# Kernel tuning notes

Measured on AMD Instinct MI355X. Metric: run time of the kernel, lower is better.

The kernel has to match this reference:

```python
import jax, jax.numpy as jnp
import numpy as np

L, D, H, HD, FF, T = 8, 1024, 16, 64, 4096, 4096
SCALE = 1.4 / np.sqrt(float(L))  # muP residual scale: scale_depth/sqrt(num_hidden_layers)
THETA, EPS = 10000.0, 1e-5


def _rms(x, w):
    return x * jax.lax.rsqrt(jnp.mean(x * x, axis=-1, keepdims=True) + EPS) * w


def _rope(x, cos, sin):
    # rotate-half RoPE on last dim; cos/sin: [HD//2]
    x1, x2 = jnp.split(x, 2, axis=-1)
    return jnp.concatenate([x1 * cos - x2 * sin, x1 * sin + x2 * cos], axis=-1)


def setup_inputs() -> dict:
    key = jax.random.key(0)
    ks = jax.random.split(key, 10)
    nrm = lambda k, shape, s=1.0: jax.random.normal(k, shape, dtype=jnp.float32) * s
    inp = {"embed": nrm(ks[0], (1, 1, D))}
    ck = jax.random.split(ks[1], 2 * L)
    for i in range(L):
        inp[f"k{i}"] = nrm(ck[2 * i], (1, H, T, HD))
        inp[f"v{i}"] = nrm(ck[2 * i + 1], (1, H, T, HD))
    inp["ln1_w"] = jnp.ones((L, D), jnp.float32)
    inp["ln2_w"] = jnp.ones((L, D), jnp.float32)
    inp["norm_w"] = jnp.ones((D,), jnp.float32)
    w = 0.02
    inp["Wq"] = nrm(ks[2], (L, D, D), w)
    inp["Wk"] = nrm(ks[3], (L, D, D), w)
    inp["Wv"] = nrm(ks[4], (L, D, D), w)
    inp["Wo"] = nrm(ks[5], (L, D, D), w)
    inp["Wg"] = nrm(ks[6], (L, D, FF), w)
    inp["Wu"] = nrm(ks[7], (L, D, FF), w)
    inp["Wd"] = nrm(ks[8], (L, FF, D), w)
    inp["position"] = T  # decode position == current cache length
    return inp


def reference(embed, position, k0, v0, k1, v1, k2, v2, k3, v3, k4, v4, k5, v5, k6, v6, k7, v7,
              ln1_w, ln2_w, norm_w, Wq, Wk, Wv, Wo, Wg, Wu, Wd):
    caches = [(k0, v0), (k1, v1), (k2, v2), (k3, v3), (k4, v4), (k5, v5), (k6, v6), (k7, v7)]
    inv_freq = 1.0 / (THETA ** (jnp.arange(0, HD, 2, dtype=jnp.float32) / HD))  # [HD//2]
    ang = jnp.asarray(position, jnp.float32) * inv_freq
    cos, sin = jnp.cos(ang), jnp.sin(ang)
    hidden = embed  # [1,1,D]
    new_caches = []
    for i in range(L):
        residual = hidden
        h = _rms(hidden, ln1_w[i])
        q = (h @ Wq[i]).reshape(1, 1, H, HD).transpose(0, 2, 1, 3)   # [1,H,1,HD]
        kn = (h @ Wk[i]).reshape(1, 1, H, HD).transpose(0, 2, 1, 3)
        vn = (h @ Wv[i]).reshape(1, 1, H, HD).transpose(0, 2, 1, 3)
        q, kn = _rope(q, cos, sin), _rope(kn, cos, sin)
        kc = jnp.concatenate([caches[i][0], kn], axis=2)  # [1,H,T+1,HD]
        vc = jnp.concatenate([caches[i][1], vn], axis=2)
        new_caches.append((kc, vc))
        scores = jnp.einsum('bhqd,bhkd->bhqk', q, kc) / np.sqrt(float(HD))
        attn = jax.nn.softmax(scores, axis=-1)
        o = jnp.einsum('bhqk,bhkd->bhqd', attn, vc).transpose(0, 2, 1, 3).reshape(1, 1, D) @ Wo[i]
        hidden = residual + o * SCALE
        residual = hidden
        h = _rms(hidden, ln2_w[i])
        m = (jax.nn.silu(h @ Wg[i]) * (h @ Wu[i])) @ Wd[i]
        hidden = residual + m * SCALE
    out = [_rms(hidden, norm_w)]
    for kc, vc in new_caches:
        out.extend([kc, vc])
    return tuple(out)
```

## Files before the change

### kernel.cpp

```cpp
#include <hip/hip_runtime.h>
#include <stdint.h>

#define D_ 1024
#define H_ 16
#define HD_ 64
#define FF_ 4096
#define T_ 4096
#define TC_ 4097
#define CHUNK_ 128
#define NCH_ 32
#define NV_ 9
#define LAYERS_ 8

#define WS_QKV 0
#define WS_GU 3072
#define WS_HID 11264
#define WS_PART 12288

static constexpr float SCALE_ = 0.49497474683058327f;
static constexpr float EPS_ = 1e-5f;

typedef float nf4 __attribute__((ext_vector_type(4)));

__device__ __forceinline__ float wave_sum(float v) {
    #pragma unroll
    for (int off = 32; off; off >>= 1) v += __shfl_down(v, off, 64);
    return v;
}
__device__ __forceinline__ float wave_max(float v) {
    #pragma unroll
    for (int off = 32; off; off >>= 1) v = fmaxf(v, __shfl_down(v, off, 64));
    return v;
}

__device__ __forceinline__ void rms_to_sm(const float* __restrict__ hid,
                                          const float* __restrict__ lnw,
                                          float* hn, float* wred, int t)
{
    float4 hv = ((const float4*)hid)[t];
    float ssq = hv.x*hv.x + hv.y*hv.y + hv.z*hv.z + hv.w*hv.w;
    ssq = wave_sum(ssq);
    if ((t & 63) == 0) wred[t >> 6] = ssq;
    __syncthreads();
    float rms = rsqrtf((wred[0] + wred[1] + wred[2] + wred[3]) * (1.0f / D_) + EPS_);
    float4 lw = ((const float4*)lnw)[t];
    hn[4*t+0] = hv.x * rms * lw.x;
    hn[4*t+1] = hv.y * rms * lw.y;
    hn[4*t+2] = hv.z * rms * lw.z;
    hn[4*t+3] = hv.w * rms * lw.w;
    __syncthreads();
}

template<int RT>
__device__ __forceinline__ void gemv_tile(const float* __restrict__ hsrc,
                                          const float* __restrict__ W, int ncols,
                                          int rowbase, int colbase, float scale,
                                          float* __restrict__ dst, float4* red4, int t)
{
    constexpr int RPG = RT / 8;
    int cg = t & 31, rg = t >> 5;
    int row0 = rowbase + rg * RPG;
    const float* Wp = W + (size_t)row0 * ncols + colbase + cg * 4;
    float4 acc = make_float4(0.f, 0.f, 0.f, 0.f);
    #pragma unroll
    for (int r = 0; r < RPG; ++r) {
        float hs = hsrc[row0 + r];
        float4 w4 = *(const float4*)(Wp + (size_t)r * ncols);
        acc.x += hs*w4.x; acc.y += hs*w4.y; acc.z += hs*w4.z; acc.w += hs*w4.w;
    }
    red4[t] = acc;
    __syncthreads();
    if (t < 32) {
        float4 s = red4[t];
        #pragma unroll
        for (int g = 1; g < 8; ++g) {
            float4 r4 = red4[t + 32*g];
            s.x += r4.x; s.y += r4.y; s.z += r4.z; s.w += r4.w;
        }
        float* d = dst + colbase + t*4;
        atomicAdd(d+0, scale*s.x);
        atomicAdd(d+1, scale*s.y);
        atomicAdd(d+2, scale*s.z);
        atomicAdd(d+3, scale*s.w);
    }
    __syncthreads();
}

__global__ void k_init(const float* __restrict__ embed, float* __restrict__ hid,
                       float* __restrict__ accQKV) {
    int t = threadIdx.x;
    ((float4*)hid)[t] = ((const float4*)embed)[t];
    for (int i = t; i < 3072; i += 256) accQKV[i] = 0.f;
}

template<int NCOLS, int RT>
__global__ void k_rms_gemv(const float* __restrict__ hidden, const float* __restrict__ lnw,
                           const float* __restrict__ W0, const float* __restrict__ W1,
                           const float* __restrict__ W2, float* __restrict__ out)
{
    int t = threadIdx.x;
    __shared__ float hn[D_];
    __shared__ float wred[4];
    __shared__ float4 red4s[256];
    rms_to_sm(hidden, lnw, hn, wred, t);
    const float* W = (blockIdx.z == 0) ? W0 : (blockIdx.z == 1 ? W1 : W2);
    gemv_tile<RT>(hn, W, NCOLS, blockIdx.y*RT, blockIdx.x*128, 1.f,
                  out + (size_t)blockIdx.z * NCOLS, red4s, t);
}

__global__ void k_attn_f(const float* __restrict__ kcache, const float* __restrict__ vcache,
                         const float* __restrict__ qkv, const int* __restrict__ posp,
                         float* __restrict__ kc_out, float* __restrict__ vc_out,
                         float* __restrict__ part)
{
    int c = blockIdx.x, h = blockIdx.y, t = threadIdx.x;
    __shared__ float qr[64], kr[64], sc[132], wr2[8];
    __shared__ float4 red4[256];
    if (t < 32) {
        float pos = (float)(*posp);
        float inv = expf(-(float)t * (9.210340371976184f / 32.0f));
        float ang = pos * inv;
        float cs = cosf(ang), sn = sinf(ang);
        float q1 = qkv[h*64 + t], q2 = qkv[h*64 + t + 32];
        qr[t] = q1*cs - q2*sn; qr[t+32] = q1*sn + q2*cs;
        float k1 = qkv[1024 + h*64 + t], k2 = qkv[1024 + h*64 + t + 32];
        kr[t] = k1*cs - k2*sn; kr[t+32] = k1*sn + k2*cs;
    }

    int kstart = c * CHUNK_;
    int nk = (c == NCH_-1) ? (TC_ - kstart) : CHUNK_;
    int d4 = (t & 15) * 4;
    int kl0 = t >> 4;

    nf4 vreg[NV_];
    #pragma unroll
    for (int j = 0; j < NV_; ++j) {
        int kl = kl0 + 16 * j;
        if (kl < nk) {
            int key = kstart + kl;
            if (key < T_)
                vreg[j] = __builtin_nontemporal_load((const nf4*)(vcache + ((size_t)h*T_ + key)*HD_ + d4));
            else
                vreg[j] = *(const nf4*)(qkv + 2048 + h*64 + d4);
        }
    }

    __syncthreads();
    nf4 qv = *(const nf4*)&qr[d4];
    #pragma unroll
    for (int j = 0; j < NV_; ++j) {
        int kl = kl0 + 16 * j;
        if (kl < nk) {
            int key = kstart + kl;
            nf4 kv;
            if (key < T_) kv = __builtin_nontemporal_load((const nf4*)(kcache + ((size_t)h*T_ + key)*HD_ + d4));
            else          kv = *(const nf4*)&kr[d4];
            float pd = qv.x*kv.x + qv.y*kv.y + qv.z*kv.z + qv.w*kv.w;
            pd += __shfl_down(pd, 8, 16);
            pd += __shfl_down(pd, 4, 16);
            pd += __shfl_down(pd, 2, 16);
            pd += __shfl_down(pd, 1, 16);
            if ((t & 15) == 0) sc[kl] = pd * 0.125f;
            __builtin_nontemporal_store(kv, (nf4*)(kc_out + ((size_t)h*TC_ + key)*HD_ + d4));
        }
    }
    #pragma unroll
    for (int j = 0; j < NV_; ++j) {
        int kl = kl0 + 16 * j;
        if (kl < nk) {
            int key = kstart + kl;
            __builtin_nontemporal_store(vreg[j], (nf4*)(vc_out + ((size_t)h*TC_ + key)*HD_ + d4));
        }
    }
    __syncthreads();
    float m = (t < nk) ? sc[t] : -INFINITY;
    m = wave_max(m);
    if ((t & 63) == 0) wr2[t >> 6] = m;
    __syncthreads();
    m = fmaxf(fmaxf(wr2[0], wr2[1]), fmaxf(wr2[2], wr2[3]));
    float e = 0.f;
    if (t < nk) { e = __expf(sc[t] - m); sc[t] = e; }
    float s = wave_sum(e);
    if ((t & 63) == 0) wr2[4 + (t >> 6)] = s;
    __syncthreads();
    float* pb = part + ((size_t)h*NCH_ + c)*66;
    if (t == 0) { pb[0] = m; pb[1] = wr2[4]+wr2[5]+wr2[6]+wr2[7]; }
    __syncthreads();
    float4 acc = make_float4(0.f, 0.f, 0.f, 0.f);
    #pragma unroll
    for (int j = 0; j < NV_; ++j) {
        int kl = kl0 + 16 * j;
        if (kl < nk) {
            float w = sc[kl];
            acc.x += w*vreg[j].x; acc.y += w*vreg[j].y;
            acc.z += w*vreg[j].z; acc.w += w*vreg[j].w;
        }
    }
    red4[t] = acc;
    __syncthreads();
    if (t < 16) {
        float4 s4 = red4[t];
        #pragma unroll
        for (int g = 1; g < 16; ++g) {
            float4 r4 = red4[t + 16*g];
            s4.x += r4.x; s4.y += r4.y; s4.z += r4.z; s4.w += r4.w;
        }
        pb[2 + t*4 + 0] = s4.x;
        pb[2 + t*4 + 1] = s4.y;
        pb[2 + t*4 + 2] = s4.z;
        pb[2 + t*4 + 3] = s4.w;
    }
}

__global__ void k_wo(const float* __restrict__ part, const float* __restrict__ Wo,
                     float* __restrict__ hidden, float* __restrict__ accGU)
{
    int h = blockIdx.y, t = threadIdx.x;
    if (blockIdx.x == 0 && blockIdx.y == 0)
        for (int i = t; i < 2*FF_; i += 256) accGU[i] = 0.f;
    __shared__ float oh[64];
    __shared__ float4 red4s[256];
    if (t < 64) {
        const float* pb = part + (size_t)h * NCH_ * 66;
        float M = -INFINITY;
        for (int c = 0; c < NCH_; ++c) M = fmaxf(M, pb[c*66]);
        float S = 0.f, O = 0.f;
        for (int c = 0; c < NCH_; ++c) {
            float e = __expf(pb[c*66] - M);
            S += pb[c*66 + 1] * e;
            O += pb[c*66 + 2 + t] * e;
        }
        oh[t] = O / S;
    }
    __syncthreads();
    gemv_tile<64>(oh - h*64, Wo, D_, h*64, blockIdx.x*128, SCALE_, hidden, red4s, t);
}

__global__ void k_down(const float* __restrict__ gu, const float* __restrict__ Wd,
                       float* __restrict__ hidden, float* __restrict__ accQKV)
{
    int t = threadIdx.x;
    if (blockIdx.x == 0 && blockIdx.y == 0)
        for (int i = t; i < 3072; i += 256) accQKV[i] = 0.f;
    __shared__ float act[128];
    __shared__ float4 red4s[256];
    int rowbase = blockIdx.y * 128;
    if (t < 128) {
        float g = gu[rowbase + t];
        float u = gu[FF_ + rowbase + t];
        act[t] = g / (1.f + __expf(-g)) * u;
    }
    __syncthreads();
    gemv_tile<128>(act - rowbase, Wd, D_, rowbase, blockIdx.x*128, SCALE_, hidden, red4s, t);
}

__global__ void k_final(const float* __restrict__ hidden, const float* __restrict__ nw,
                        float* __restrict__ out)
{
    int t = threadIdx.x;
    __shared__ float wred[4];
    float4 hv = ((const float4*)hidden)[t];
    float ssq = hv.x*hv.x + hv.y*hv.y + hv.z*hv.z + hv.w*hv.w;
    ssq = wave_sum(ssq);
    if ((t & 63) == 0) wred[t >> 6] = ssq;
    __syncthreads();
    float rms = rsqrtf((wred[0] + wred[1] + wred[2] + wred[3]) * (1.0f / D_) + EPS_);
    float4 w = ((const float4*)nw)[t];
    float4 ob;
    ob.x = hv.x * rms * w.x; ob.y = hv.y * rms * w.y;
    ob.z = hv.z * rms * w.z; ob.w = hv.w * rms * w.w;
    ((float4*)out)[t] = ob;
}

static const int ROLE_SIZES[28] = {
    1024,
    4194304,4194304,4194304,4194304,4194304,4194304,4194304,4194304,
    4194304,4194304,4194304,4194304,4194304,4194304,4194304,4194304,
    8192, 8192, 1024,
    8388608, 8388608, 8388608, 8388608,
    33554432, 33554432, 33554432,
    1
};

extern "C" void kernel_launch(void* const* d_in, const int* in_sizes, int n_in,
                              void* d_out, int out_size, void* d_ws, size_t ws_size,
                              hipStream_t stream)
{
    int perm[28];
    bool matched = false;
    auto try_perm = [&](const int* cand) {
        if (matched) return;
        for (int r = 0; r < 28; ++r)
            if (in_sizes[cand[r]] != ROLE_SIZES[r]) return;
        for (int r = 0; r < 28; ++r) perm[r] = cand[r];
        matched = true;
    };
    {   int c[28]; for (int r = 0; r < 28; ++r) c[r] = r; try_perm(c); }
    {   int c[28];
        c[0]=0; c[27]=1;
        for (int i = 0; i < 8; ++i) { c[1+2*i]=2+2*i; c[2+2*i]=3+2*i; }
        c[17]=18; c[18]=19; c[19]=20;
        c[20]=21; c[21]=22; c[22]=23; c[23]=24; c[24]=25; c[25]=26; c[26]=27;
        try_perm(c); }
    if (!matched) { for (int r = 0; r < 28; ++r) perm[r] = r; }

    const float* embed = (const float*)d_in[perm[0]];
    const float* kcs[LAYERS_];
    const float* vcs[LAYERS_];
    for (int i = 0; i < LAYERS_; ++i) {
        kcs[i] = (const float*)d_in[perm[1+2*i]];
        vcs[i] = (const float*)d_in[perm[2+2*i]];
    }
    const float* ln1 = (const float*)d_in[perm[17]];
    const float* ln2 = (const float*)d_in[perm[18]];
    const float* nw  = (const float*)d_in[perm[19]];
    const float* Wq  = (const float*)d_in[perm[20]];
    const float* Wk  = (const float*)d_in[perm[21]];
    const float* Wv  = (const float*)d_in[perm[22]];
    const float* Wo  = (const float*)d_in[perm[23]];
    const float* Wg  = (const float*)d_in[perm[24]];
    const float* Wu  = (const float*)d_in[perm[25]];
    const float* Wd  = (const float*)d_in[perm[26]];
    const int*   pos = (const int*)d_in[perm[27]];

    float* out = (float*)d_out;
    float* ws = (float*)d_ws;
    float* accQKV = ws + WS_QKV;
    float* accGU  = ws + WS_GU;
    float* hid    = ws + WS_HID;
    float* part   = ws + WS_PART;

    (void)out_size; (void)ws_size; (void)n_in;

    k_init<<<1, 256, 0, stream>>>(embed, hid, accQKV);

    const size_t KVSZ = (size_t)H_ * TC_ * HD_;
    for (int i = 0; i < LAYERS_; ++i) {
        float* kco = out + 1024 + (size_t)i * 2 * KVSZ;
        float* vco = kco + KVSZ;

        k_rms_gemv<D_, 64><<<dim3(8, 16, 3), 256, 0, stream>>>(
            hid, ln1 + i*D_,
            Wq + (size_t)i*D_*D_, Wk + (size_t)i*D_*D_, Wv + (size_t)i*D_*D_,
            accQKV);

        k_attn_f<<<dim3(NCH_, H_), 256, 0, stream>>>(kcs[i], vcs[i], accQKV, pos,
                                                     kco, vco, part);

        k_wo<<<dim3(8, 16), 256, 0, stream>>>(part, Wo + (size_t)i*D_*D_, hid, accGU);

        k_rms_gemv<FF_, 128><<<dim3(32, 8, 2), 256, 0, stream>>>(
            hid, ln2 + i*D_,
            Wg + (size_t)i*D_*FF_, Wu + (size_t)i*D_*FF_, nullptr,
            accGU);

        k_down<<<dim3(8, 32), 256, 0, stream>>>(accGU, Wd + (size_t)i*FF_*D_, hid, accQKV);
    }
    k_final<<<1, 256, 0, stream>>>(hid, nw, out);
}
```

Baseline: 372.6 us.

## Move KV cache copy-out into extra blocks of the GEMV kernels

The attention kernel no longer writes the whole old K/V cache to the output. It only writes the new token's row. The bulk copy of the old cache is split into halves and done by extra blocks appended to the QKV, Wo, gate/up and down GEMV launches. The aim is to overlap this bandwidth-bound copy with the weight-streaming GEMVs, which use few blocks, and to cut store traffic from the attention kernel. In exchange the copy blocks compete for HBM bandwidth with the weight reads, and the extra blocks in each launch add some launch cost.

Result: slower. 503.7 us (+35.2%).

```diff
diff --git a/kernel.cpp b/kernel.cpp
--- a/kernel.cpp
+++ b/kernel.cpp
@@ -17,6 +17,10 @@
 #define WS_HID 11264
 #define WS_PART 12288
 
+#define HEAD_F4 65536
+#define DSTH_F4 65552
+#define HALF_F4 524288
+
 static constexpr float SCALE_ = 0.49497474683058327f;
 static constexpr float EPS_ = 1e-5f;
 
@@ -31,6 +35,19 @@
     #pragma unroll
     for (int off = 32; off; off >>= 1) v = fmaxf(v, __shfl_down(v, off, 64));
     return v;
+}
+
+__device__ __forceinline__ void copy_kv(const float* __restrict__ src, float* __restrict__ dst,
+                                        int base4, int rank, int cpb, int t)
+{
+    long i0 = (long)base4 + (long)rank * cpb;
+    for (int j = t; j < cpb; j += 256) {
+        long i4 = i0 + j;
+        int h = (int)(i4 >> 16);
+        long rem = i4 & (HEAD_F4 - 1);
+        nf4 v = __builtin_nontemporal_load((const nf4*)src + i4);
+        __builtin_nontemporal_store(v, (nf4*)dst + (long)h * DSTH_F4 + rem);
+    }
 }
 
 __device__ __forceinline__ void rms_to_sm(const float* __restrict__ hid,
@@ -93,12 +110,17 @@
     for (int i = t; i < 3072; i += 256) accQKV[i] = 0.f;
 }
 
-template<int NCOLS, int RT>
+template<int NCOLS, int RT, int NZ, int CPB>
 __global__ void k_rms_gemv(const float* __restrict__ hidden, const float* __restrict__ lnw,
                            const float* __restrict__ W0, const float* __restrict__ W1,
-                           const float* __restrict__ W2, float* __restrict__ out)
-{
-    int t = threadIdx.x;
+                           const float* __restrict__ W2, float* __restrict__ out,
+                           const float* __restrict__ csrc, float* __restrict__ cdst, int cbase4)
+{
+    int t = threadIdx.x;
+    if (blockIdx.z == NZ) {
+        copy_kv(csrc, cdst, cbase4, blockIdx.y * gridDim.x + blockIdx.x, CPB, t);
+        return;
+    }
     __shared__ float hn[D_];
     __shared__ float wred[4];
     __shared__ float4 red4s[256];
@@ -138,10 +160,12 @@
         int kl = kl0 + 16 * j;
         if (kl < nk) {
             int key = kstart + kl;
-            if (key < T_)
+            if (key < T_) {
                 vreg[j] = __builtin_nontemporal_load((const nf4*)(vcache + ((size_t)h*T_ + key)*HD_ + d4));
-            else
+            } else {
                 vreg[j] = *(const nf4*)(qkv + 2048 + h*64 + d4);
+                __builtin_nontemporal_store(vreg[j], (nf4*)(vc_out + ((size_t)h*TC_ + key)*HD_ + d4));
+            }
         }
     }
 
@@ -153,23 +177,18 @@
         if (kl < nk) {
             int key = kstart + kl;
             nf4 kv;
-            if (key < T_) kv = __builtin_nontemporal_load((const nf4*)(kcache + ((size_t)h*T_ + key)*HD_ + d4));
-            else          kv = *(const nf4*)&kr[d4];
+            if (key < T_) {
+                kv = __builtin_nontemporal_load((const nf4*)(kcache + ((size_t)h*T_ + key)*HD_ + d4));
+            } else {
+                kv = *(const nf4*)&kr[d4];
+                __builtin_nontemporal_store(kv, (nf4*)(kc_out + ((size_t)h*TC_ + key)*HD_ + d4));
+            }
             float pd = qv.x*kv.x + qv.y*kv.y + qv.z*kv.z + qv.w*kv.w;
             pd += __shfl_down(pd, 8, 16);
             pd += __shfl_down(pd, 4, 16);
             pd += __shfl_down(pd, 2, 16);
             pd += __shfl_down(pd, 1, 16);
             if ((t & 15) == 0) sc[kl] = pd * 0.125f;
-            __builtin_nontemporal_store(kv, (nf4*)(kc_out + ((size_t)h*TC_ + key)*HD_ + d4));
-        }
-    }
-    #pragma unroll
-    for (int j = 0; j < NV_; ++j) {
-        int kl = kl0 + 16 * j;
-        if (kl < nk) {
-            int key = kstart + kl;
-            __builtin_nontemporal_store(vreg[j], (nf4*)(vc_out + ((size_t)h*TC_ + key)*HD_ + d4));
         }
     }
     __syncthreads();
@@ -213,9 +232,15 @@
 }
 
 __global__ void k_wo(const float* __restrict__ part, const float* __restrict__ Wo,
-                     float* __restrict__ hidden, float* __restrict__ accGU)
-{
-    int h = blockIdx.y, t = threadIdx.x;
+                     float* __restrict__ hidden, float* __restrict__ accGU,
+                     const float* __restrict__ csrc, float* __restrict__ cdst, int cbase4)
+{
+    int t = threadIdx.x;
+    if (blockIdx.y >= 16) {
+        copy_kv(csrc, cdst, cbase4, (blockIdx.y - 16) * 8 + blockIdx.x, 4096, t);
+        return;
+    }
+    int h = blockIdx.y;
     if (blockIdx.x == 0 && blockIdx.y == 0)
         for (int i = t; i < 2*FF_; i += 256) accGU[i] = 0.f;
     __shared__ float oh[64];
@@ -237,9 +262,14 @@
 }
 
 __global__ void k_down(const float* __restrict__ gu, const float* __restrict__ Wd,
-                       float* __restrict__ hidden, float* __restrict__ accQKV)
-{
-    int t = threadIdx.x;
+                       float* __restrict__ hidden, float* __restrict__ accQKV,
+                       const float* __restrict__ csrc, float* __restrict__ cdst, int cbase4)
+{
+    int t = threadIdx.x;
+    if (blockIdx.y >= 32) {
+        copy_kv(csrc, cdst, cbase4, (blockIdx.y - 32) * 8 + blockIdx.x, 4096, t);
+        return;
+    }
     if (blockIdx.x == 0 && blockIdx.y == 0)
         for (int i = t; i < 3072; i += 256) accQKV[i] = 0.f;
     __shared__ float act[128];
@@ -339,22 +369,24 @@
         float* kco = out + 1024 + (size_t)i * 2 * KVSZ;
         float* vco = kco + KVSZ;
 
-        k_rms_gemv<D_, 64><<<dim3(8, 16, 3), 256, 0, stream>>>(
+        k_rms_gemv<D_, 64, 3, 4096><<<dim3(8, 16, 4), 256, 0, stream>>>(
             hid, ln1 + i*D_,
             Wq + (size_t)i*D_*D_, Wk + (size_t)i*D_*D_, Wv + (size_t)i*D_*D_,
-            accQKV);
+            accQKV, kcs[i], kco, 0);
 
         k_attn_f<<<dim3(NCH_, H_), 256, 0, stream>>>(kcs[i], vcs[i], accQKV, pos,
                                                      kco, vco, part);
 
-        k_wo<<<dim3(8, 16), 256, 0, stream>>>(part, Wo + (size_t)i*D_*D_, hid, accGU);
-
-        k_rms_gemv<FF_, 128><<<dim3(32, 8, 2), 256, 0, stream>>>(
+        k_wo<<<dim3(8, 32), 256, 0, stream>>>(part, Wo + (size_t)i*D_*D_, hid, accGU,
+                                              kcs[i], kco, HALF_F4);
+
+        k_rms_gemv<FF_, 128, 2, 2048><<<dim3(32, 8, 3), 256, 0, stream>>>(
             hid, ln2 + i*D_,
             Wg + (size_t)i*D_*FF_, Wu + (size_t)i*D_*FF_, nullptr,
-            accGU);
-
-        k_down<<<dim3(8, 32), 256, 0, stream>>>(accGU, Wd + (size_t)i*FF_*D_, hid, accQKV);
+            accGU, vcs[i], vco, 0);
+
+        k_down<<<dim3(8, 48), 256, 0, stream>>>(accGU, Wd + (size_t)i*FF_*D_, hid, accQKV,
+                                                vcs[i], vco, HALF_F4);
     }
     k_final<<<1, 256, 0, stream>>>(hid, nw, out);
 }
```
